# Kernel optimization log

Hardware: AMD Instinct MI355X
Metric: run time of the kernel (lower is better)

## Reference

```python
import jax, jax.numpy as jnp
import numpy as np


def _dequantize(qweight, scale, zero_point, bits, group_size):
    """Unpack int32-packed weights and apply group-wise dequantization.

    qweight:    [N, K // (32//bits)] int32, value i within an int32 at shift i*bits
    scale/zp:   [N, K // group_size]
    returns W:  [N, K] float32
    """
    vpi = 32 // bits  # values per int32
    mask = (1 << bits) - 1
    N, packed = qweight.shape
    K = packed * vpi
    shifts = (jnp.arange(vpi, dtype=jnp.int32) * bits)  # [vpi]
    # [N, packed, vpi] -> flatten so value i of each int32 lands at consecutive K positions
    q = (qweight[:, :, None] >> shifts[None, None, :]) & mask
    q = q.reshape(N, K // group_size, group_size).astype(jnp.float32)
    w = scale[:, :, None] * (q - zero_point[:, :, None])  # group-wise dequant
    return w.reshape(N, K)


def setup_inputs() -> dict:
    key = jax.random.key(0)
    k1, k2, k3, k4, k5 = jax.random.split(key, 5)
    B, S, K, N = 4, 2048, 4096, 4096
    bits, group_size = 4, 128
    vpi = 32 // bits
    num_groups = K // group_size
    x = jax.random.normal(k1, (B, S, K), dtype=jnp.float32)
    qweight = jax.random.randint(k2, (N, K // vpi), jnp.iinfo(jnp.int32).min,
                                 jnp.iinfo(jnp.int32).max, dtype=jnp.int32)
    scale = jax.random.uniform(k3, (N, num_groups), dtype=jnp.float32,
                               minval=0.001, maxval=0.02)
    zero_point = jax.random.uniform(k4, (N, num_groups), dtype=jnp.float32,
                                    minval=0.0, maxval=float((1 << bits) - 1))
    bias = jax.random.normal(k5, (N,), dtype=jnp.float32)
    return {"x": x, "qweight": qweight, "scale": scale, "zero_point": zero_point,
            "bias": bias, "bits": bits, "group_size": group_size}


def reference(x, qweight, scale, zero_point, bias, bits, group_size):
    # Fused dequant + GEMM: y = x @ W^T + b, W dequantized from packed int4 groups
    w = _dequantize(qweight, scale, zero_point, bits, group_size)  # [N, K]
    y = jnp.einsum('bsk,nk->bsn', x, w)
    return y + bias
```

## Files before the change

### kernel.cpp

```cpp
#include <hip/hip_runtime.h>

#define KD 4096
#define ND 4096
#define GRP 32
#define NT (KD / 64)

typedef unsigned short u16;
typedef float   f32x4  __attribute__((ext_vector_type(4)));
typedef __bf16  bf16x8 __attribute__((ext_vector_type(8)));
typedef unsigned short u16x8 __attribute__((ext_vector_type(8)));
typedef unsigned short u16x4 __attribute__((ext_vector_type(4)));

__device__ __forceinline__ u16 f2bf(float f) {
  unsigned u = __float_as_uint(f);
  return (u16)((u + 0x7fffu + ((u >> 16) & 1u)) >> 16);
}

__device__ __forceinline__ void async16(const void* g, void* l) {
  __builtin_amdgcn_global_load_lds(
      (const __attribute__((address_space(1))) unsigned int*)g,
      (__attribute__((address_space(3))) unsigned int*)l, 16, 0, 0);
}

__global__ __launch_bounds__(256) void prep_kernel(
    const int* __restrict__ qw, const float* __restrict__ scale,
    const float* __restrict__ zp, u16* __restrict__ wout,
    const float4* __restrict__ x, u16x4* __restrict__ xb, int nx) {
  const int nth = gridDim.x * 256;
  const int t0 = blockIdx.x * 256 + threadIdx.x;
  for (int idx4 = t0; idx4 < ND * (KD / 32); idx4 += nth) {
    int n = idx4 >> 7;
    int p4 = idx4 & 127;
    int g = p4 >> 2;
    float s = scale[n * GRP + g];
    float bz = -s * zp[n * GRP + g];
    int4 q4 = ((const int4*)qw)[idx4];
    const unsigned qv[4] = {(unsigned)q4.x, (unsigned)q4.y,
                            (unsigned)q4.z, (unsigned)q4.w};
#pragma unroll
    for (int k = 0; k < 4; ++k) {
      u16x8 hv;
#pragma unroll
      for (int i = 0; i < 8; ++i)
        hv[i] = f2bf(fmaf((float)((qv[k] >> (4 * i)) & 15u), s, bz));
      *(u16x8*)(wout + (size_t)idx4 * 32 + k * 8) = hv;
    }
  }
  for (int i = t0; i < nx; i += nth) {
    float4 v = x[i];
    u16x4 h;
    h[0] = f2bf(v.x); h[1] = f2bf(v.y); h[2] = f2bf(v.z); h[3] = f2bf(v.w);
    xb[i] = h;
  }
}

__global__ __launch_bounds__(512, 2) void gemm256(
    const u16* __restrict__ xb, const u16* __restrict__ wb,
    const float* __restrict__ bias, float* __restrict__ out) {
  __shared__ u16 As[2][256 * 64];
  __shared__ u16 Bs[2][256 * 64];
  const int tid = threadIdx.x;
  const int l = tid & 63, w = tid >> 6;
  const int wr = w >> 2, wc = w & 3;
  const int col = l & 15, quad = l >> 4, rsw = col & 7;
  const int lr = l >> 3, csrc = (l & 7) ^ lr;

  const int id = blockIdx.y * gridDim.x + blockIdx.x;
  const int nwg = gridDim.x * gridDim.y;
  const int q = nwg >> 3, r = nwg & 7;
  const int xcd = id & 7, off = id >> 3;
  const int wgid = (xcd < r ? xcd * (q + 1) : r * (q + 1) + (xcd - r) * q) + off;
  const int nb = gridDim.x;
  const int m0 = (wgid / nb) * 256;
  const int n0 = (wgid % nb) * 256;

  const u16* asrc = xb + (size_t)(m0 + w * 16 + lr) * KD + csrc * 8;
  const u16* bsrc = wb + (size_t)(n0 + w * 16 + lr) * KD + csrc * 8;

#define STAGE_A(t, h)                                                      \
  do {                                                                     \
    const u16* _g = asrc + (size_t)((h) * 128) * KD + (t) * 64;            \
    u16* _l = &As[(t) & 1][((h) * 128 + w * 16) * 64];                     \
    async16(_g, _l);                                                       \
    async16(_g + (size_t)8 * KD, _l + 8 * 64);                             \
  } while (0)
#define STAGE_B(t, h)                                                      \
  do {                                                                     \
    const u16* _g = bsrc + (size_t)((h) * 128) * KD + (t) * 64;            \
    u16* _l = &Bs[(t) & 1][((h) * 128 + w * 16) * 64];                     \
    async16(_g, _l);                                                       \
    async16(_g + (size_t)8 * KD, _l + 8 * 64);                             \
  } while (0)
#define STAGE4(t) do { STAGE_B(t, 0); STAGE_B(t, 1); STAGE_A(t, 0); STAGE_A(t, 1); } while (0)
#define BAR()   __builtin_amdgcn_s_barrier()
#define SB0()   __builtin_amdgcn_sched_barrier(0)
#define LDA(Ab, i, kk) \
  (*(const bf16x8*)&(Ab)[(wr * 128 + (i) * 16 + col) * 64 + ((((kk) * 4 + quad) ^ rsw) * 8)])
#define LDB(Bb, j, kk) \
  (*(const bf16x8*)&(Bb)[(wc * 64 + (j) * 16 + col) * 64 + ((((kk) * 4 + quad) ^ rsw) * 8)])
#define COMPUTE(Ab, Bb)                                                    \
  do {                                                                     \
    _Pragma("unroll")                                                      \
    for (int i = 0; i < 4; ++i) { a[i][0] = LDA(Ab, i, 0); a[i][1] = LDA(Ab, i, 1); } \
    _Pragma("unroll")                                                      \
    for (int j = 0; j < 4; ++j) { b[j][0] = LDB(Bb, j, 0); b[j][1] = LDB(Bb, j, 1); } \
    _Pragma("unroll")                                                      \
    for (int kk = 0; kk < 2; ++kk)                                         \
      _Pragma("unroll")                                                    \
      for (int i = 0; i < 4; ++i)                                          \
        _Pragma("unroll")                                                  \
        for (int j = 0; j < 4; ++j)                                        \
          acc[i][j] = __builtin_amdgcn_mfma_f32_16x16x32_bf16(             \
              a[i][kk], b[j][kk], acc[i][j], 0, 0, 0);                     \
    _Pragma("unroll")                                                      \
    for (int i = 0; i < 4; ++i) { a[i][0] = LDA(Ab, i + 4, 0); a[i][1] = LDA(Ab, i + 4, 1); } \
    _Pragma("unroll")                                                      \
    for (int kk = 0; kk < 2; ++kk)                                         \
      _Pragma("unroll")                                                    \
      for (int i = 0; i < 4; ++i)                                          \
        _Pragma("unroll")                                                  \
        for (int j = 0; j < 4; ++j)                                        \
          acc[4 + i][j] = __builtin_amdgcn_mfma_f32_16x16x32_bf16(         \
              a[i][kk], b[j][kk], acc[4 + i][j], 0, 0, 0);                 \
  } while (0)
#define DRAIN() do { asm volatile("s_waitcnt vmcnt(0)"); SB0(); BAR(); } while (0)

  f32x4 acc[8][4] = {};
  bf16x8 a[4][2], b[4][2];

  STAGE4(0);
  DRAIN();

  for (int tt = 0; tt < NT - 2; tt += 2) {
    STAGE4(tt + 1);
    SB0();
    COMPUTE(As[0], Bs[0]);
    DRAIN();
    STAGE4(tt + 2);
    SB0();
    COMPUTE(As[1], Bs[1]);
    DRAIN();
  }
  STAGE4(NT - 1);
  SB0();
  COMPUTE(As[0], Bs[0]);
  DRAIN();
  COMPUTE(As[1], Bs[1]);

#pragma unroll
  for (int j = 0; j < 4; ++j) {
    int n = n0 + wc * 64 + j * 16 + col;
    float bj = bias[n];
#pragma unroll
    for (int i = 0; i < 8; ++i) {
      int mrow = m0 + wr * 128 + i * 16 + quad * 4;
#pragma unroll
      for (int rr = 0; rr < 4; ++rr)
        out[(size_t)(mrow + rr) * ND + n] = acc[i][j][rr] + bj;
    }
  }
#undef STAGE_A
#undef STAGE_B
#undef STAGE4
#undef BAR
#undef SB0
#undef LDA
#undef LDB
#undef COMPUTE
#undef DRAIN
}

template <int XF32, int WQ>
__global__ __launch_bounds__(256, 3) void gemm_kernel(
    const u16*   __restrict__ xbp,
    const float* __restrict__ xf,
    const u16*   __restrict__ wbp,
    const int*   __restrict__ qw,
    const float* __restrict__ scale,
    const float* __restrict__ zp,
    const float* __restrict__ bias,
    float* __restrict__ out) {
  __shared__ u16 As[128 * 64];
  __shared__ u16 Bs[128 * 64];
  const int tid = threadIdx.x;
  const int l = tid & 63, w = tid >> 6;
  const int m0 = blockIdx.y * 128, n0 = blockIdx.x * 128;
  const int wm = (w >> 1) * 64, wn = (w & 1) * 64;
  const int col = l & 15, quad = l >> 4;
  const int rsw = col & 7;
  const int lr = l >> 3;
  const int csrc = (l & 7) ^ lr;
  f32x4 acc[4][4] = {};

  for (int k0 = 0; k0 < KD; k0 += 64) {
    __syncthreads();

    if constexpr (XF32) {
#pragma unroll
      for (int it = 0; it < 8; ++it) {
        int fi = it * 256 + tid;
        int row = fi >> 4, cs = fi & 15;
        float4 v = *(const float4*)(xf + (size_t)(m0 + row) * KD + k0 + cs * 4);
        u16x4 h;
        h[0] = f2bf(v.x); h[1] = f2bf(v.y); h[2] = f2bf(v.z); h[3] = f2bf(v.w);
        int slot = (cs >> 1) ^ (row & 7);
        *(u16x4*)(&As[row * 64 + slot * 8 + (cs & 1) * 4]) = h;
      }
    } else {
#pragma unroll
      for (int c = 0; c < 4; ++c) {
        int br = w * 32 + c * 8;
        const u16* g = xbp + (size_t)(m0 + br + lr) * KD + k0 + csrc * 8;
        async16(g, &As[br * 64]);
      }
    }

    if constexpr (WQ) {
#pragma unroll
      for (int it = 0; it < 4; ++it) {
        int qi = it * 256 + tid;
        int row = qi >> 3, p8 = qi & 7;
        int nrow = n0 + row;
        int g = k0 >> 7;
        float s = scale[nrow * GRP + g];
        float bz = -s * zp[nrow * GRP + g];
        unsigned qv = (unsigned)qw[(size_t)nrow * (KD / 8) + (k0 >> 3) + p8];
        u16x8 hv;
#pragma unroll
        for (int i = 0; i < 8; ++i)
          hv[i] = f2bf(fmaf((float)((qv >> (4 * i)) & 15u), s, bz));
        *(u16x8*)(&Bs[row * 64 + ((p8 ^ (row & 7)) * 8)]) = hv;
      }
    } else {
#pragma unroll
      for (int c = 0; c < 4; ++c) {
        int br = w * 32 + c * 8;
        const u16* g = wbp + (size_t)(n0 + br + lr) * KD + k0 + csrc * 8;
        async16(g, &Bs[br * 64]);
      }
    }

    __syncthreads();

#pragma unroll
    for (int kk = 0; kk < 2; ++kk) {
      bf16x8 a[4], b[4];
      const int slot = ((kk * 4 + quad) ^ rsw) * 8;
#pragma unroll
      for (int i = 0; i < 4; ++i)
        a[i] = *(const bf16x8*)&As[(wm + i * 16 + col) * 64 + slot];
#pragma unroll
      for (int j = 0; j < 4; ++j)
        b[j] = *(const bf16x8*)&Bs[(wn + j * 16 + col) * 64 + slot];
#pragma unroll
      for (int i = 0; i < 4; ++i)
#pragma unroll
        for (int j = 0; j < 4; ++j)
          acc[i][j] = __builtin_amdgcn_mfma_f32_16x16x32_bf16(a[i], b[j], acc[i][j], 0, 0, 0);
    }
  }

#pragma unroll
  for (int j = 0; j < 4; ++j) {
    int n = n0 + wn + j * 16 + col;
    float bj = bias[n];
#pragma unroll
    for (int i = 0; i < 4; ++i) {
      int mrow = m0 + wm + i * 16 + quad * 4;
#pragma unroll
      for (int rr = 0; rr < 4; ++rr)
        out[(size_t)(mrow + rr) * ND + n] = acc[i][j][rr] + bj;
    }
  }
}

extern "C" void kernel_launch(void* const* d_in, const int* in_sizes, int n_in,
                              void* d_out, int out_size, void* d_ws, size_t ws_size,
                              hipStream_t stream) {
  const float* x     = (const float*)d_in[0];
  const int*   qw    = (const int*)d_in[1];
  const float* scale = (const float*)d_in[2];
  const float* zp    = (const float*)d_in[3];
  const float* bias  = (const float*)d_in[4];
  float* out = (float*)d_out;

  const int M = in_sizes[0] / KD;

  const size_t needW = (size_t)ND * KD * sizeof(u16);
  const size_t needX = (size_t)M * KD * sizeof(u16);

  if (ws_size >= needW + needX && (M % 256) == 0) {
    u16* wb = (u16*)d_ws;
    u16* xbuf = wb + (size_t)ND * KD;
    prep_kernel<<<2048, 256, 0, stream>>>(qw, scale, zp, wb,
                                          (const float4*)x, (u16x4*)xbuf,
                                          M * (KD / 4));
    dim3 grid(ND / 256, M / 256);
    gemm256<<<grid, dim3(512), 0, stream>>>(xbuf, wb, bias, out);
  } else if (ws_size >= needW) {
    u16* wb = (u16*)d_ws;
    prep_kernel<<<2048, 256, 0, stream>>>(qw, scale, zp, wb, nullptr, nullptr, 0);
    dim3 grid(ND / 128, M / 128);
    gemm_kernel<1, 0><<<grid, dim3(256), 0, stream>>>(nullptr, x, wb, qw, scale, zp, bias, out);
  } else {
    dim3 grid(ND / 128, M / 128);
    gemm_kernel<1, 1><<<grid, dim3(256), 0, stream>>>(nullptr, x, nullptr, qw, scale, zp, bias, out);
  }
}
```

Baseline: 480.1 us.

## Use 4 waves with 128x128 per-wave tiles in gemm256

Restructures the 256x256 GEMM block from 8 waves (each computing 128x64) to 4 waves each computing a 128x128 sub-tile with an 8x8 accumulator array. Each wave now stages 64 rows of A and B per k-step, and the compute loop reloads A and B fragments per kk step. The intent is better LDS reuse per MFMA with fewer LDS reads per flop and fewer waves to synchronize. In exchange register pressure rises sharply (256 accumulator VGPRs), occupancy drops to one 256-thread block per CU, and there are fewer waves available to hide latency.

```diff
diff --git a/kernel.cpp b/kernel.cpp
--- a/kernel.cpp
+++ b/kernel.cpp
@@ -54,14 +54,14 @@
   }
 }
 
-__global__ __launch_bounds__(512, 2) void gemm256(
+__global__ __launch_bounds__(256, 1) void gemm256(
     const u16* __restrict__ xb, const u16* __restrict__ wb,
     const float* __restrict__ bias, float* __restrict__ out) {
   __shared__ u16 As[2][256 * 64];
   __shared__ u16 Bs[2][256 * 64];
   const int tid = threadIdx.x;
   const int l = tid & 63, w = tid >> 6;
-  const int wr = w >> 2, wc = w & 3;
+  const int wr = w >> 1, wc = w & 1;
   const int col = l & 15, quad = l >> 4, rsw = col & 7;
   const int lr = l >> 3, csrc = (l & 7) ^ lr;
 
@@ -74,82 +74,68 @@
   const int m0 = (wgid / nb) * 256;
   const int n0 = (wgid % nb) * 256;
 
-  const u16* asrc = xb + (size_t)(m0 + w * 16 + lr) * KD + csrc * 8;
-  const u16* bsrc = wb + (size_t)(n0 + w * 16 + lr) * KD + csrc * 8;
-
-#define STAGE_A(t, h)                                                      \
+  const u16* asrc = xb + (size_t)(m0 + w * 64 + lr) * KD + csrc * 8;
+  const u16* bsrc = wb + (size_t)(n0 + w * 64 + lr) * KD + csrc * 8;
+
+#define STAGE(t)                                                           \
   do {                                                                     \
-    const u16* _g = asrc + (size_t)((h) * 128) * KD + (t) * 64;            \
-    u16* _l = &As[(t) & 1][((h) * 128 + w * 16) * 64];                     \
-    async16(_g, _l);                                                       \
-    async16(_g + (size_t)8 * KD, _l + 8 * 64);                             \
+    _Pragma("unroll")                                                      \
+    for (int c = 0; c < 8; ++c) {                                          \
+      async16(asrc + (size_t)(c * 8) * KD + (t) * 64,                      \
+              &As[(t) & 1][(w * 64 + c * 8) * 64]);                        \
+      async16(bsrc + (size_t)(c * 8) * KD + (t) * 64,                      \
+              &Bs[(t) & 1][(w * 64 + c * 8) * 64]);                        \
+    }                                                                      \
   } while (0)
-#define STAGE_B(t, h)                                                      \
-  do {                                                                     \
-    const u16* _g = bsrc + (size_t)((h) * 128) * KD + (t) * 64;            \
-    u16* _l = &Bs[(t) & 1][((h) * 128 + w * 16) * 64];                     \
-    async16(_g, _l);                                                       \
-    async16(_g + (size_t)8 * KD, _l + 8 * 64);                             \
-  } while (0)
-#define STAGE4(t) do { STAGE_B(t, 0); STAGE_B(t, 1); STAGE_A(t, 0); STAGE_A(t, 1); } while (0)
 #define BAR()   __builtin_amdgcn_s_barrier()
 #define SB0()   __builtin_amdgcn_sched_barrier(0)
 #define LDA(Ab, i, kk) \
   (*(const bf16x8*)&(Ab)[(wr * 128 + (i) * 16 + col) * 64 + ((((kk) * 4 + quad) ^ rsw) * 8)])
 #define LDB(Bb, j, kk) \
-  (*(const bf16x8*)&(Bb)[(wc * 64 + (j) * 16 + col) * 64 + ((((kk) * 4 + quad) ^ rsw) * 8)])
+  (*(const bf16x8*)&(Bb)[(wc * 128 + (j) * 16 + col) * 64 + ((((kk) * 4 + quad) ^ rsw) * 8)])
 #define COMPUTE(Ab, Bb)                                                    \
   do {                                                                     \
     _Pragma("unroll")                                                      \
-    for (int i = 0; i < 4; ++i) { a[i][0] = LDA(Ab, i, 0); a[i][1] = LDA(Ab, i, 1); } \
-    _Pragma("unroll")                                                      \
-    for (int j = 0; j < 4; ++j) { b[j][0] = LDB(Bb, j, 0); b[j][1] = LDB(Bb, j, 1); } \
-    _Pragma("unroll")                                                      \
-    for (int kk = 0; kk < 2; ++kk)                                         \
+    for (int kk = 0; kk < 2; ++kk) {                                       \
       _Pragma("unroll")                                                    \
-      for (int i = 0; i < 4; ++i)                                          \
+      for (int j = 0; j < 8; ++j) b[j] = LDB(Bb, j, kk);                   \
+      _Pragma("unroll")                                                    \
+      for (int i = 0; i < 8; ++i) a[i] = LDA(Ab, i, kk);                   \
+      _Pragma("unroll")                                                    \
+      for (int i = 0; i < 8; ++i)                                          \
         _Pragma("unroll")                                                  \
-        for (int j = 0; j < 4; ++j)                                        \
+        for (int j = 0; j < 8; ++j)                                        \
           acc[i][j] = __builtin_amdgcn_mfma_f32_16x16x32_bf16(             \
-              a[i][kk], b[j][kk], acc[i][j], 0, 0, 0);                     \
-    _Pragma("unroll")                                                      \
-    for (int i = 0; i < 4; ++i) { a[i][0] = LDA(Ab, i + 4, 0); a[i][1] = LDA(Ab, i + 4, 1); } \
-    _Pragma("unroll")                                                      \
-    for (int kk = 0; kk < 2; ++kk)                                         \
-      _Pragma("unroll")                                                    \
-      for (int i = 0; i < 4; ++i)                                          \
-        _Pragma("unroll")                                                  \
-        for (int j = 0; j < 4; ++j)                                        \
-          acc[4 + i][j] = __builtin_amdgcn_mfma_f32_16x16x32_bf16(         \
-              a[i][kk], b[j][kk], acc[4 + i][j], 0, 0, 0);                 \
+              a[i], b[j], acc[i][j], 0, 0, 0);                             \
+    }                                                                      \
   } while (0)
 #define DRAIN() do { asm volatile("s_waitcnt vmcnt(0)"); SB0(); BAR(); } while (0)
 
-  f32x4 acc[8][4] = {};
-  bf16x8 a[4][2], b[4][2];
-
-  STAGE4(0);
+  f32x4 acc[8][8] = {};
+  bf16x8 a[8], b[8];
+
+  STAGE(0);
   DRAIN();
 
   for (int tt = 0; tt < NT - 2; tt += 2) {
-    STAGE4(tt + 1);
+    STAGE(tt + 1);
     SB0();
     COMPUTE(As[0], Bs[0]);
     DRAIN();
-    STAGE4(tt + 2);
+    STAGE(tt + 2);
     SB0();
     COMPUTE(As[1], Bs[1]);
     DRAIN();
   }
-  STAGE4(NT - 1);
+  STAGE(NT - 1);
   SB0();
   COMPUTE(As[0], Bs[0]);
   DRAIN();
   COMPUTE(As[1], Bs[1]);
 
 #pragma unroll
-  for (int j = 0; j < 4; ++j) {
-    int n = n0 + wc * 64 + j * 16 + col;
+  for (int j = 0; j < 8; ++j) {
+    int n = n0 + wc * 128 + j * 16 + col;
     float bj = bias[n];
 #pragma unroll
     for (int i = 0; i < 8; ++i) {
@@ -159,9 +145,7 @@
         out[(size_t)(mrow + rr) * ND + n] = acc[i][j][rr] + bj;
     }
   }
-#undef STAGE_A
-#undef STAGE_B
-#undef STAGE4
+#undef STAGE
 #undef BAR
 #undef SB0
 #undef LDA
@@ -296,7 +280,7 @@
                                           (const float4*)x, (u16x4*)xbuf,
                                           M * (KD / 4));
     dim3 grid(ND / 256, M / 256);
-    gemm256<<<grid, dim3(512), 0, stream>>>(xbuf, wb, bias, out);
+    gemm256<<<grid, dim3(256), 0, stream>>>(xbuf, wb, bias, out);
   } else if (ws_size >= needW) {
     u16* wb = (u16*)d_ws;
     prep_kernel<<<2048, 256, 0, stream>>>(qw, scale, zp, wb, nullptr, nullptr, 0);
```

After: 607.7 us. 1.27x slower.
